# Kernel optimization log

Measured on AMD Instinct MI355X. Metric: run time of the kernel, lower is better.

## Reference

```python
import jax, jax.numpy as jnp
import numpy as np

WIDTH_IN = 8
WIDTH_OUT = 8
STRIDES = (1, 1)
PADDING = 'SAME'


def quantizer(x, width, mode='round', clip=True):
    """Fixed-point quantization to `width` bits in [-1, 1), straight-through estimator.

    mode='round' -> round-to-nearest; mode='floor' -> truncate.
    clip=True saturates to the representable range [-1, 1 - 2^-(width-1)].
    """
    scale = jnp.asarray(2.0 ** (width - 1), x.dtype)
    q = jnp.round(x * scale) if mode == 'round' else jnp.floor(x * scale)
    q = q / scale
    # straight-through: forward uses q, gradient flows as identity
    q = x + jax.lax.stop_gradient(q - x)
    if clip:
        q = jnp.clip(q, -1.0, 1.0 - 1.0 / scale)
    return q


def setup_inputs() -> dict:
    key = jax.random.key(0)
    kx, kw = jax.random.split(key)
    x = jax.random.normal(kx, (32, 112, 112, 64), dtype=jnp.float32)      # NHWC
    kernels = jax.random.normal(kw, (3, 3, 64, 128), dtype=jnp.float32) * 0.05  # HWIO, RandomNormal init
    return {"x": x, "kernels": kernels}


def reference(x, kernels):
    # Method == 'Fixed' path of MyConv2D.call
    xq = quantizer(x, WIDTH_IN, 'round', clip=True)                # quantize activations
    kq = quantizer(kernels, WIDTH_IN, 'round', clip=True)          # quantize weights
    out = jax.lax.conv_general_dilated(
        xq, kq,
        window_strides=STRIDES,
        padding=PADDING,
        dimension_numbers=('NHWC', 'HWIO', 'NHWC'),
    )                                                              # [B, 112, 112, 128]
    out = quantizer(out, WIDTH_OUT, 'floor', clip=False)           # quantize output, truncating
    return out
```

## Files before the change

### kernel.cpp

```cpp
#include <hip/hip_runtime.h>

#define NIMG 32
#define H 112
#define W 112
#define CI 64
#define CO 128

typedef __attribute__((ext_vector_type(8))) __bf16 bf16x8;
typedef __attribute__((ext_vector_type(4))) float f32x4;
typedef __attribute__((ext_vector_type(4))) short short4v;
typedef __attribute__((ext_vector_type(4))) int int4v;
typedef __attribute__((ext_vector_type(2))) int int2v;

__device__ __forceinline__ short q8bits(float v) {
    float t = rintf(v * 128.0f);
    t = fminf(fmaxf(t, -128.0f), 127.0f);
    union { float f; unsigned u; } cv; cv.f = t;
    return (short)(cv.u >> 16);
}
__device__ __forceinline__ int q8i(float v) {
    float t = rintf(v * 128.0f);
    t = fminf(fmaxf(t, -128.0f), 127.0f);
    return (int)t;
}

__global__ __launch_bounds__(256) void quant_pack_w_i8(const float* __restrict__ w,
                                                       signed char* __restrict__ bp) {
    int idx = blockIdx.x * 256 + threadIdx.x;
    int j  = idx & 15;
    int l  = (idx >> 4) & 63;
    int nt = (idx >> 10) & 7;
    int kk = idx >> 13;
    int k = kk * 64 + (l >> 4) * 16 + j;
    int n = nt * 16 + (l & 15);
    bp[idx] = (signed char)q8i(w[k * CO + n]);
}

__global__ __launch_bounds__(256) void quant_x_i8(const float* __restrict__ x,
                                                  signed char* __restrict__ xq) {
    size_t i = ((size_t)blockIdx.x * 256 + threadIdx.x) * 8;
    float4 v0 = *(const float4*)&x[i];
    float4 v1 = *(const float4*)&x[i + 4];
    int b0 = (q8i(v0.x) & 255) | ((q8i(v0.y) & 255) << 8) |
             ((q8i(v0.z) & 255) << 16) | (q8i(v0.w) << 24);
    int b1 = (q8i(v1.x) & 255) | ((q8i(v1.y) & 255) << 8) |
             ((q8i(v1.z) & 255) << 16) | (q8i(v1.w) << 24);
    int2v p; p.x = b0; p.y = b1;
    *(int2v*)&xq[i] = p;
}

#define RB 7296

__global__ __launch_bounds__(256) void conv_i8(const signed char* __restrict__ xq,
                                               const signed char* __restrict__ bp,
                                               float* __restrict__ out) {
    __shared__ __align__(16) signed char xs[3 * RB];
    int bid0 = blockIdx.x;
    int bid = (bid0 & 7) * 448 + (bid0 >> 3);
    int n = bid / H;
    int h = bid - n * H;
    int tid  = threadIdx.x;
    int lane = tid & 63;
    int wave = tid >> 6;

    const signed char* base = xq + (size_t)(n * H) * (W * CI);
    for (int idx = wave; idx < 21; idx += 4) {
        int row = idx / 7;
        int i = idx - row * 7;
        int hr = h - 1 + row;
        if ((unsigned)hr < (unsigned)H) {
            const signed char* g = base + (size_t)hr * (W * CI) + i * 1024 + lane * 16;
            __builtin_amdgcn_global_load_lds(
                (const __attribute__((address_space(1))) void*)g,
                (__attribute__((address_space(3))) void*)(xs + row * RB + 64 + i * 1024),
                16, 0, 0);
        }
    }

    if (h == 0)
        for (int t = tid; t < 456; t += 256) *(int4v*)&xs[t * 16] = (int4v){0, 0, 0, 0};
    if (h == H - 1)
        for (int t = tid; t < 456; t += 256) *(int4v*)&xs[2 * RB + t * 16] = (int4v){0, 0, 0, 0};
    if (tid < 24) {
        int r2 = tid >> 3, ci = tid & 7;
        int c = (ci & 4) ? 113 : 0;
        *(int4v*)&xs[r2 * RB + c * 64 + (ci & 3) * 16] = (int4v){0, 0, 0, 0};
    }
    __syncthreads();

    int lane15 = lane & 15;
    int hi     = lane >> 4;
    int nt0    = wave * 2;
    const int4v* bp4 = (const int4v*)bp;

    int4v acc[7][2];
    #pragma unroll
    for (int mt = 0; mt < 7; ++mt) {
        acc[mt][0] = (int4v){0, 0, 0, 0};
        acc[mt][1] = (int4v){0, 0, 0, 0};
    }

    #pragma unroll
    for (int r = 0; r < 3; ++r) {
        #pragma unroll
        for (int s = 0; s < 3; ++s) {
            int kk = r * 3 + s;
            int4v b0 = bp4[(kk * 8 + nt0    ) * 64 + lane];
            int4v b1 = bp4[(kk * 8 + nt0 + 1) * 64 + lane];
            int abase = r * RB + (s + lane15) * 64 + hi * 16;
            #pragma unroll
            for (int mt = 0; mt < 7; ++mt) {
                int4v a = *(const int4v*)&xs[abase + mt * 1024];
                acc[mt][0] = __builtin_amdgcn_mfma_i32_16x16x64_i8(a, b0, acc[mt][0], 0, 0, 0);
                acc[mt][1] = __builtin_amdgcn_mfma_i32_16x16x64_i8(a, b1, acc[mt][1], 0, 0, 0);
            }
        }
    }

    float* orow = out + (size_t)((n * H + h) * W) * CO;
    int co0  = wave * 32 + lane15;
    int rowb = hi * 4;
    #pragma unroll
    for (int mt = 0; mt < 7; ++mt)
        #pragma unroll
        for (int t = 0; t < 2; ++t)
            #pragma unroll
            for (int rg = 0; rg < 4; ++rg) {
                int m = mt * 16 + rowb + rg;
                orow[m * CO + co0 + t * 16] =
                    (float)(acc[mt][t][rg] >> 7) * 0.0078125f;
            }
}

__global__ __launch_bounds__(256) void quant_pack_w(const float* __restrict__ w,
                                                    short* __restrict__ bp) {
    int idx = blockIdx.x * 256 + threadIdx.x;
    int j    = idx & 7;
    int lane = (idx >> 3) & 63;
    int nt   = (idx >> 9) & 7;
    int kt   = idx >> 12;
    int k = kt * 32 + (lane >> 4) * 8 + j;
    int n = nt * 16 + (lane & 15);
    bp[idx] = q8bits(w[k * CO + n]);
}

#define LDSW 114
#define LDST 72
__global__ __launch_bounds__(256) void conv_fb(const float* __restrict__ x,
                                               const short* __restrict__ bp,
                                               float* __restrict__ out) {
    __shared__ short xs[3 * LDSW * LDST];
    int bid = blockIdx.x;
    int n = bid / H;
    int h = bid - n * H;
    int tid = threadIdx.x;
    const float* xin = x + (size_t)n * (H * W * CI);
    for (int r = 0; r < 3; ++r) {
        int hrow = h + r - 1;
        bool rowok = ((unsigned)hrow < (unsigned)H);
        const float* srow = xin + (size_t)hrow * (W * CI);
        for (int t = tid; t < LDSW * 16; t += 256) {
            int c = t >> 4;
            int ci4 = (t & 15) << 2;
            int wcol = c - 1;
            float4 v = {0.f, 0.f, 0.f, 0.f};
            if (rowok && (unsigned)wcol < (unsigned)W)
                v = *(const float4*)&srow[wcol * CI + ci4];
            short4v sv;
            sv.x = q8bits(v.x); sv.y = q8bits(v.y);
            sv.z = q8bits(v.z); sv.w = q8bits(v.w);
            *(short4v*)&xs[(r * LDSW + c) * LDST + ci4] = sv;
        }
    }
    __syncthreads();
    int lane = tid & 63;
    int wave = tid >> 6;
    int laneoff = (lane & 15) * LDST + (lane >> 4) * 8;
    const bf16x8* bfr = (const bf16x8*)bp;
    int nt0 = wave * 2;
    f32x4 acc[7][2];
    #pragma unroll
    for (int mt = 0; mt < 7; ++mt) {
        acc[mt][0] = (f32x4){0.f, 0.f, 0.f, 0.f};
        acc[mt][1] = (f32x4){0.f, 0.f, 0.f, 0.f};
    }
    #pragma unroll
    for (int kk = 0; kk < 18; ++kk) {
        int rs = kk >> 1;
        int r = rs / 3;
        int s = rs - r * 3;
        bf16x8 b0 = bfr[(kk * 8 + nt0    ) * 64 + lane];
        bf16x8 b1 = bfr[(kk * 8 + nt0 + 1) * 64 + lane];
        int abase = (r * LDSW + s) * LDST + (kk & 1) * 32 + laneoff;
        #pragma unroll
        for (int mt = 0; mt < 7; ++mt) {
            bf16x8 a = *(const bf16x8*)&xs[abase + mt * 16 * LDST];
            acc[mt][0] = __builtin_amdgcn_mfma_f32_16x16x32_bf16(a, b0, acc[mt][0], 0, 0, 0);
            acc[mt][1] = __builtin_amdgcn_mfma_f32_16x16x32_bf16(a, b1, acc[mt][1], 0, 0, 0);
        }
    }
    float* orow = out + (size_t)(n * H + h) * (W * CO);
    int colc = wave * 32 + (lane & 15);
    int rowb = (lane >> 4) * 4;
    #pragma unroll
    for (int mt = 0; mt < 7; ++mt)
        #pragma unroll
        for (int t2 = 0; t2 < 2; ++t2)
            #pragma unroll
            for (int rg = 0; rg < 4; ++rg) {
                int m = mt * 16 + rowb + rg;
                orow[m * CO + colc + t2 * 16] =
                    floorf(acc[mt][t2][rg] * 0.0078125f) * 0.0078125f;
            }
}

extern "C" void kernel_launch(void* const* d_in, const int* in_sizes, int n_in,
                              void* d_out, int out_size, void* d_ws, size_t ws_size,
                              hipStream_t stream) {
    const float* x = (const float*)d_in[0];
    const float* w = (const float*)d_in[1];
    float* out = (float*)d_out;

    const size_t BPI8_BYTES = 73728;
    const size_t XQ8_BYTES  = (size_t)NIMG * H * W * CI;

    if (ws_size >= BPI8_BYTES + XQ8_BYTES) {
        signed char* bp8 = (signed char*)d_ws;
        signed char* xq8 = (signed char*)d_ws + BPI8_BYTES;
        quant_pack_w_i8<<<288, 256, 0, stream>>>(w, bp8);
        quant_x_i8<<<12544, 256, 0, stream>>>(x, xq8);
        conv_i8<<<NIMG * H, 256, 0, stream>>>(xq8, bp8, out);
    } else {
        short* bp = (short*)d_ws;
        quant_pack_w<<<288, 256, 0, stream>>>(w, bp);
        conv_fb<<<NIMG * H, 256, 0, stream>>>(x, bp, out);
    }
}
```

Before: 301.9 us.

## Fuse input quantization into int8 conv and compute two output rows per block

```diff
diff --git a/kernel.cpp b/kernel.cpp
--- a/kernel.cpp
+++ b/kernel.cpp
@@ -5,12 +5,12 @@
 #define W 112
 #define CI 64
 #define CO 128
+#define GP2 56
 
 typedef __attribute__((ext_vector_type(8))) __bf16 bf16x8;
 typedef __attribute__((ext_vector_type(4))) float f32x4;
 typedef __attribute__((ext_vector_type(4))) short short4v;
 typedef __attribute__((ext_vector_type(4))) int int4v;
-typedef __attribute__((ext_vector_type(2))) int int2v;
 
 __device__ __forceinline__ short q8bits(float v) {
     float t = rintf(v * 128.0f);
@@ -36,55 +36,45 @@
     bp[idx] = (signed char)q8i(w[k * CO + n]);
 }
 
-__global__ __launch_bounds__(256) void quant_x_i8(const float* __restrict__ x,
-                                                  signed char* __restrict__ xq) {
-    size_t i = ((size_t)blockIdx.x * 256 + threadIdx.x) * 8;
-    float4 v0 = *(const float4*)&x[i];
-    float4 v1 = *(const float4*)&x[i + 4];
-    int b0 = (q8i(v0.x) & 255) | ((q8i(v0.y) & 255) << 8) |
-             ((q8i(v0.z) & 255) << 16) | (q8i(v0.w) << 24);
-    int b1 = (q8i(v1.x) & 255) | ((q8i(v1.y) & 255) << 8) |
-             ((q8i(v1.z) & 255) << 16) | (q8i(v1.w) << 24);
-    int2v p; p.x = b0; p.y = b1;
-    *(int2v*)&xq[i] = p;
-}
-
 #define RB 7296
 
-__global__ __launch_bounds__(256) void conv_i8(const signed char* __restrict__ xq,
-                                               const signed char* __restrict__ bp,
-                                               float* __restrict__ out) {
-    __shared__ __align__(16) signed char xs[3 * RB];
+__global__ __launch_bounds__(256) void conv_i8f(const float* __restrict__ x,
+                                                const signed char* __restrict__ bp,
+                                                float* __restrict__ out) {
+    __shared__ __align__(16) signed char xs[4 * RB];
     int bid0 = blockIdx.x;
-    int bid = (bid0 & 7) * 448 + (bid0 >> 3);
-    int n = bid / H;
-    int h = bid - n * H;
+    int bid = (bid0 & 7) * 224 + (bid0 >> 3);
+    int n = bid / GP2;
+    int g = bid - n * GP2;
+    int h0 = g * 2;
     int tid  = threadIdx.x;
     int lane = tid & 63;
     int wave = tid >> 6;
 
-    const signed char* base = xq + (size_t)(n * H) * (W * CI);
-    for (int idx = wave; idx < 21; idx += 4) {
-        int row = idx / 7;
-        int i = idx - row * 7;
-        int hr = h - 1 + row;
+    if (tid < 32)
+        *(int4v*)&xs[(tid >> 3) * RB + ((tid & 4) ? 113 : 0) * 64 + (tid & 3) * 16] =
+            (int4v){0, 0, 0, 0};
+
+    #pragma unroll
+    for (int r = 0; r < 4; ++r) {
+        int hr = h0 - 1 + r;
+        signed char* dst = &xs[r * RB + 64];
         if ((unsigned)hr < (unsigned)H) {
-            const signed char* g = base + (size_t)hr * (W * CI) + i * 1024 + lane * 16;
-            __builtin_amdgcn_global_load_lds(
-                (const __attribute__((address_space(1))) void*)g,
-                (__attribute__((address_space(3))) void*)(xs + row * RB + 64 + i * 1024),
-                16, 0, 0);
-        }
-    }
-
-    if (h == 0)
-        for (int t = tid; t < 456; t += 256) *(int4v*)&xs[t * 16] = (int4v){0, 0, 0, 0};
-    if (h == H - 1)
-        for (int t = tid; t < 456; t += 256) *(int4v*)&xs[2 * RB + t * 16] = (int4v){0, 0, 0, 0};
-    if (tid < 24) {
-        int r2 = tid >> 3, ci = tid & 7;
-        int c = (ci & 4) ? 113 : 0;
-        *(int4v*)&xs[r2 * RB + c * 64 + (ci & 3) * 16] = (int4v){0, 0, 0, 0};
+            const float* src = x + ((size_t)(n * H + hr) * W) * CI;
+            float4 v[7];
+            #pragma unroll
+            for (int k = 0; k < 7; ++k) v[k] = *(const float4*)&src[k * 1024 + tid * 4];
+            #pragma unroll
+            for (int k = 0; k < 7; ++k) {
+                int b = (q8i(v[k].x) & 255) | ((q8i(v[k].y) & 255) << 8) |
+                        ((q8i(v[k].z) & 255) << 16) | (q8i(v[k].w) << 24);
+                *(int*)&dst[k * 1024 + tid * 4] = b;
+            }
+        } else {
+            #pragma unroll
+            for (int k = 0; k < 7; ++k)
+                *(int*)&dst[k * 1024 + tid * 4] = 0;
+        }
     }
     __syncthreads();
 
@@ -93,43 +83,47 @@
     int nt0    = wave * 2;
     const int4v* bp4 = (const int4v*)bp;
 
-    int4v acc[7][2];
-    #pragma unroll
-    for (int mt = 0; mt < 7; ++mt) {
-        acc[mt][0] = (int4v){0, 0, 0, 0};
-        acc[mt][1] = (int4v){0, 0, 0, 0};
-    }
-
-    #pragma unroll
-    for (int r = 0; r < 3; ++r) {
-        #pragma unroll
-        for (int s = 0; s < 3; ++s) {
-            int kk = r * 3 + s;
-            int4v b0 = bp4[(kk * 8 + nt0    ) * 64 + lane];
-            int4v b1 = bp4[(kk * 8 + nt0 + 1) * 64 + lane];
-            int abase = r * RB + (s + lane15) * 64 + hi * 16;
-            #pragma unroll
-            for (int mt = 0; mt < 7; ++mt) {
-                int4v a = *(const int4v*)&xs[abase + mt * 1024];
-                acc[mt][0] = __builtin_amdgcn_mfma_i32_16x16x64_i8(a, b0, acc[mt][0], 0, 0, 0);
-                acc[mt][1] = __builtin_amdgcn_mfma_i32_16x16x64_i8(a, b1, acc[mt][1], 0, 0, 0);
+    #pragma unroll
+    for (int trow = 0; trow < 2; ++trow) {
+        int4v acc[7][2];
+        #pragma unroll
+        for (int mt = 0; mt < 7; ++mt) {
+            acc[mt][0] = (int4v){0, 0, 0, 0};
+            acc[mt][1] = (int4v){0, 0, 0, 0};
+        }
+
+        #pragma unroll
+        for (int r = 0; r < 3; ++r) {
+            int sbase = (trow + r) * RB;
+            #pragma unroll
+            for (int s = 0; s < 3; ++s) {
+                int kk = r * 3 + s;
+                int4v b0 = bp4[(kk * 8 + nt0    ) * 64 + lane];
+                int4v b1 = bp4[(kk * 8 + nt0 + 1) * 64 + lane];
+                int abase = sbase + (s + lane15) * 64 + hi * 16;
+                #pragma unroll
+                for (int mt = 0; mt < 7; ++mt) {
+                    int4v a = *(const int4v*)&xs[abase + mt * 1024];
+                    acc[mt][0] = __builtin_amdgcn_mfma_i32_16x16x64_i8(a, b0, acc[mt][0], 0, 0, 0);
+                    acc[mt][1] = __builtin_amdgcn_mfma_i32_16x16x64_i8(a, b1, acc[mt][1], 0, 0, 0);
+                }
             }
         }
-    }
-
-    float* orow = out + (size_t)((n * H + h) * W) * CO;
-    int co0  = wave * 32 + lane15;
-    int rowb = hi * 4;
-    #pragma unroll
-    for (int mt = 0; mt < 7; ++mt)
-        #pragma unroll
-        for (int t = 0; t < 2; ++t)
-            #pragma unroll
-            for (int rg = 0; rg < 4; ++rg) {
-                int m = mt * 16 + rowb + rg;
-                orow[m * CO + co0 + t * 16] =
-                    (float)(acc[mt][t][rg] >> 7) * 0.0078125f;
-            }
+
+        float* orow = out + (size_t)((n * H + h0 + trow) * W) * CO;
+        int co0  = wave * 32 + lane15;
+        int rowb = hi * 4;
+        #pragma unroll
+        for (int mt = 0; mt < 7; ++mt)
+            #pragma unroll
+            for (int t = 0; t < 2; ++t)
+                #pragma unroll
+                for (int rg = 0; rg < 4; ++rg) {
+                    int m = mt * 16 + rowb + rg;
+                    orow[m * CO + co0 + t * 16] =
+                        (float)(acc[mt][t][rg] >> 7) * 0.0078125f;
+                }
+    }
 }
 
 __global__ __launch_bounds__(256) void quant_pack_w(const float* __restrict__ w,
@@ -222,14 +216,11 @@
     float* out = (float*)d_out;
 
     const size_t BPI8_BYTES = 73728;
-    const size_t XQ8_BYTES  = (size_t)NIMG * H * W * CI;
-
-    if (ws_size >= BPI8_BYTES + XQ8_BYTES) {
+
+    if (ws_size >= BPI8_BYTES) {
         signed char* bp8 = (signed char*)d_ws;
-        signed char* xq8 = (signed char*)d_ws + BPI8_BYTES;
         quant_pack_w_i8<<<288, 256, 0, stream>>>(w, bp8);
-        quant_x_i8<<<12544, 256, 0, stream>>>(x, xq8);
-        conv_i8<<<NIMG * H, 256, 0, stream>>>(xq8, bp8, out);
+        conv_i8f<<<NIMG * GP2, 256, 0, stream>>>(x, bp8, out);
     } else {
         short* bp = (short*)d_ws;
         quant_pack_w<<<288, 256, 0, stream>>>(w, bp);
```

New measurement: 305.4 us. About the same (+1.2%).
